# Kernel optimization log

Measured on AMD Instinct MI355X. Metric: run time of the kernel, lower is better.

## Reference

```python
import jax, jax.numpy as jnp
import numpy as np

N = 20000   # genes
E = 200000  # global edges
P = 300     # pathways
EP = 2000   # edges per pathway (global node indices)
D = 3       # in_dim == number of omics (forced by nn.Linear(3,1))


def setup_inputs():
    key = jax.random.key(0)
    ks = jax.random.split(key, 20)
    f = lambda i, shape: jax.random.normal(ks[i], shape, dtype=jnp.float32) * 0.1
    return {
        "x": f(0, (N, D)),
        "edge_index": jax.random.randint(ks[1], (2, E), 0, N),
        "path_edges": jax.random.randint(ks[2], (P, 2, EP), 0, N),
        "W_pool": f(3, (D, D)), "b_pool": f(4, (D,)),
        "W_self": f(5, (D, D)), "W_neigh": f(6, (D, D)), "b_conv": f(7, (D,)),
        "sub_Wl": f(8, (P, D, D)), "sub_bl": f(9, (P, D)), "sub_Wr": f(10, (P, D, D)),
        "pool_Wrel": f(11, (P, D, 1)), "pool_Wroot": f(12, (P, D, 1)), "pool_b": f(13, (P, 1)),
        "gate_W": f(14, (P, D, 1)), "gate_b": f(15, (P, 1)),
        "lin_W": f(16, (D, 1)), "lin_b": f(17, (1,)),
        "mlp_W": f(18, (P, 1)), "mlp_b": f(19, (1,)),
    }


def reference(x, edge_index, path_edges, W_pool, b_pool, W_self, W_neigh, b_conv,
              sub_Wl, sub_bl, sub_Wr, pool_Wrel, pool_Wroot, pool_b,
              gate_W, gate_b, lin_W, lin_b, mlp_W, mlp_b):
    n = x.shape[0]
    # add_self_loops on the global edge_index
    loops = jnp.arange(n)
    src = jnp.concatenate([edge_index[0], loops])
    dst = jnp.concatenate([edge_index[1], loops])

    # global SAGEConv with 'pool' aggregator: max_j relu(W_pool h_j), then self + neigh
    hp = jax.nn.relu(x @ W_pool + b_pool)                       # [N,D]
    agg = jax.ops.segment_max(hp[src], dst, num_segments=n)     # [N,D] (self-loops -> no empty segments)
    h = jnp.tanh(x @ W_self + agg @ W_neigh + b_conv)           # [N,D]

    k = int(np.ceil(0.8 * n))  # SAGPooling ratio=0.8 over all N nodes (full x is passed per pathway)

    def per_path(pe, Wl, bl, Wr, Wrel, Wroot, pb, gW, gb):
        s, d = pe[0], pe[1]
        # SAGEConv (mean aggr) on pathway subgraph edges over full node set
        msum = jax.ops.segment_sum(h[s], d, num_segments=n)
        cnt = jax.ops.segment_sum(jnp.ones(s.shape, h.dtype), d, num_segments=n)
        mean = msum / jnp.maximum(cnt, 1.0)[:, None]
        xc = jax.nn.relu(mean @ Wl + bl + h @ Wr)               # [N,D]
        # SAGPooling score via GraphConv (add aggr): W_rel * sum_j x_j + W_root * x + b
        asum = jax.ops.segment_sum(xc[s], d, num_segments=n)
        score = (asum @ Wrel + xc @ Wroot + pb)[:, 0]           # [N]
        topv, perm = jax.lax.top_k(score, k)
        xk = xc[perm] * jnp.tanh(topv)[:, None]                 # [k,D]
        # GlobalAttention readout: softmax gate over kept nodes
        gate = jax.nn.softmax((xk @ gW + gb)[:, 0])             # [k]
        return jax.nn.relu(gate @ xk)                            # [D]

    readout = jax.vmap(per_path)(path_edges, sub_Wl, sub_bl, sub_Wr,
                                 pool_Wrel, pool_Wroot, pool_b, gate_W, gate_b)  # [P,D]
    r = jax.nn.relu(readout @ lin_W + lin_b).T                  # [1,P]
    # mlp: Dropout (identity in eval) -> ReLU -> Linear(P,1) -> Sigmoid
    return jax.nn.sigmoid(jax.nn.relu(r) @ mlp_W + mlp_b)       # [1,1]
```

## Files before the change

### kernel.cpp

```cpp
#include <hip/hip_runtime.h>
#include <math.h>

#define MAXM 2048
#define BMW  640
#define BS   1024
#define NB   2048

__device__ __forceinline__ unsigned fkey(float f){
  unsigned u = __float_as_uint(f);
  return (u & 0x80000000u) ? ~u : (u | 0x80000000u);
}
__device__ __forceinline__ int lbin(float sc, float lo, float scl){
  int b = (int)((sc - lo) * scl);
  return b < 0 ? 0 : (b > NB-1 ? NB-1 : b);
}
__device__ __forceinline__ float fast_tanh(float x){
  float e = __expf(2.f*x);
  return 1.f - 2.f*__builtin_amdgcn_rcpf(e + 1.f);
}
__device__ __forceinline__ void hp_eval(const float* __restrict__ x, int i,
                                        const float* __restrict__ Wp,
                                        const float* __restrict__ bp, float* o){
  float x0 = x[i*3+0], x1 = x[i*3+1], x2 = x[i*3+2];
  #pragma unroll
  for (int j = 0; j < 3; ++j)
    o[j] = fmaxf(x0*Wp[0*3+j] + x1*Wp[1*3+j] + x2*Wp[2*3+j] + bp[j], 0.f);
}

__global__ void k_edge(const float* __restrict__ x, const int* __restrict__ ei,
                       const float* __restrict__ Wp, const float* __restrict__ bp,
                       float* __restrict__ agg, float* __restrict__ acc,
                       unsigned* __restrict__ counter, int E){
  if (blockIdx.x == 0 && threadIdx.x == 0){ acc[0] = 0.f; counter[0] = 0u; }
  int e = blockIdx.x*blockDim.x + threadIdx.x;
  if (e >= E) return;
  int s = ei[e], d = ei[E+e];
  float o[3]; hp_eval(x, s, Wp, bp, o);
  #pragma unroll
  for (int j = 0; j < 3; ++j)
    if (o[j] > 0.f && o[j] > agg[d*3+j])
      atomicMax((int*)&agg[d*3+j], __float_as_int(o[j]));
}

__global__ void k_h2(const float* __restrict__ x, float* __restrict__ hb,
                     const float* __restrict__ Wp, const float* __restrict__ bp,
                     const float* __restrict__ Ws, const float* __restrict__ Wn,
                     const float* __restrict__ bc, int N){
  int i = blockIdx.x*blockDim.x + threadIdx.x;
  if (i >= N) return;
  float hp[3]; hp_eval(x, i, Wp, bp, hp);
  float x0 = x[i*3+0], x1 = x[i*3+1], x2 = x[i*3+2];
  float a0 = fmaxf(hb[i*3+0], hp[0]);
  float a1 = fmaxf(hb[i*3+1], hp[1]);
  float a2 = fmaxf(hb[i*3+2], hp[2]);
  float o[3];
  #pragma unroll
  for (int j = 0; j < 3; ++j){
    float v = x0*Ws[0*3+j] + x1*Ws[1*3+j] + x2*Ws[2*3+j]
            + a0*Wn[0*3+j] + a1*Wn[1*3+j] + a2*Wn[2*3+j] + bc[j];
    o[j] = tanhf(v);
  }
  hb[i*3+0] = o[0]; hb[i*3+1] = o[1]; hb[i*3+2] = o[2];
}

__global__ void __launch_bounds__(BS)
k_mega(const float* __restrict__ h, const int* __restrict__ pe,
       const float* __restrict__ sWl, const float* __restrict__ sbl, const float* __restrict__ sWr,
       const float* __restrict__ pWrel, const float* __restrict__ pWroot, const float* __restrict__ pB,
       const float* __restrict__ gW, const float* __restrict__ gB,
       const float* __restrict__ linW, const float* __restrict__ linb,
       const float* __restrict__ mlpW, const float* __restrict__ mlpb,
       float* __restrict__ spG, float* __restrict__ acc, unsigned* __restrict__ counter,
       unsigned* __restrict__ out, int N, int EP, int K, int P){
  __shared__ unsigned bm[BMW];
  __shared__ int      wpfx[BMW];
  __shared__ float    msum[MAXM*3];
  __shared__ unsigned scrA[NB];
  __shared__ unsigned scrB[NB];
  __shared__ unsigned candIdx[NB];
  __shared__ float    wredf[(BS/64)*2];
  __shared__ float    wredA[(BS/64)*4];
  __shared__ float    wredB[(BS/64)*4];
  __shared__ float    s_mn, s_mx;
  __shared__ float    rlo[3], rsc[3];
  __shared__ int      rb[3];
  __shared__ int      s_r, s_C, s_cc, s_done, s_fused;
  __shared__ unsigned s_uT;

  const int p = blockIdx.x;
  const int tid = threadIdx.x;

  float Wl[9], Wr[9], bl[3], wrel[3], wroot[3], gw[3];
  #pragma unroll
  for (int j = 0; j < 9; ++j){ Wl[j] = sWl[p*9+j]; Wr[j] = sWr[p*9+j]; }
  #pragma unroll
  for (int j = 0; j < 3; ++j){
    bl[j] = sbl[p*3+j]; wrel[j] = pWrel[p*3+j];
    wroot[j] = pWroot[p*3+j]; gw[j] = gW[p*3+j];
  }
  float pbv = pB[p], gbv = gB[p];
  float* sp = spG + (size_t)p*N;

  int*   cnt  = (int*)scrA;
  float* adot = (float*)scrB;

  for (int s = tid; s < MAXM; s += BS){
    cnt[s] = 0; adot[s] = 0.f;
    msum[s*3+0]=0.f; msum[s*3+1]=0.f; msum[s*3+2]=0.f;
  }
  for (int s = tid; s < BMW; s += BS) bm[s] = 0u;
  if (tid == 0){ s_done = 0; s_fused = 0; s_uT = 0u; }
  __syncthreads();

  const int* ps = pe + (size_t)p*2*EP;
  const int* pd = ps + EP;

  for (int e = tid; e < EP; e += BS) atomicOr(&bm[pd[e]>>5], 1u << (pd[e]&31));
  __syncthreads();
  if (tid < 64){
    int l = tid, base = l*10;
    int c[10], s = 0;
    #pragma unroll
    for (int q = 0; q < 10; ++q){ c[q] = __popc(bm[base+q]); s += c[q]; }
    int pre = s;
    #pragma unroll
    for (int off = 1; off < 64; off <<= 1){
      int t = __shfl_up(pre, off);
      if (l >= off) pre += t;
    }
    pre -= s;
    #pragma unroll
    for (int q = 0; q < 10; ++q){ wpfx[base+q] = pre; pre += c[q]; }
  }
  __syncthreads();
  for (int e = tid; e < EP; e += BS){
    int s = ps[e], d = pd[e];
    int r = wpfx[d>>5] + __popc(bm[d>>5] & ((1u << (d&31)) - 1u));
    atomicAdd(&cnt[r], 1);
    atomicAdd(&msum[r*3+0], h[s*3+0]);
    atomicAdd(&msum[r*3+1], h[s*3+1]);
    atomicAdd(&msum[r*3+2], h[s*3+2]);
  }
  __syncthreads();
  for (int r = tid; r < MAXM; r += BS){
    int c = cnt[r];
    if (c > 0){
      float inv = 1.f / (float)c;
      msum[r*3+0] *= inv; msum[r*3+1] *= inv; msum[r*3+2] *= inv;
    }
  }
  __syncthreads();
  for (int e = tid; e < EP; e += BS){
    int s = ps[e], d = pd[e];
    float m0=0.f,m1=0.f,m2=0.f;
    unsigned w = bm[s>>5];
    if ((w >> (s&31)) & 1u){
      int rs = wpfx[s>>5] + __popc(w & ((1u << (s&31)) - 1u));
      m0 = msum[rs*3+0]; m1 = msum[rs*3+1]; m2 = msum[rs*3+2];
    }
    float h0 = h[s*3+0], h1 = h[s*3+1], h2 = h[s*3+2];
    float x0 = fmaxf(m0*Wl[0]+m1*Wl[3]+m2*Wl[6] + bl[0] + h0*Wr[0]+h1*Wr[3]+h2*Wr[6], 0.f);
    float x1 = fmaxf(m0*Wl[1]+m1*Wl[4]+m2*Wl[7] + bl[1] + h0*Wr[1]+h1*Wr[4]+h2*Wr[7], 0.f);
    float x2 = fmaxf(m0*Wl[2]+m1*Wl[5]+m2*Wl[8] + bl[2] + h0*Wr[2]+h1*Wr[5]+h2*Wr[8], 0.f);
    int rd = wpfx[d>>5] + __popc(bm[d>>5] & ((1u << (d&31)) - 1u));
    atomicAdd(&adot[rd], x0*wrel[0] + x1*wrel[1] + x2*wrel[2]);
  }
  __syncthreads();

  float mn = 3.0e38f, mx = -3.0e38f;
  float tl = 0.f, ta0 = 0.f, ta1 = 0.f, ta2 = 0.f;
  for (int i = tid; i < N; i += BS){
    float m0=0.f,m1=0.f,m2=0.f,ad=0.f;
    unsigned w = bm[i>>5];
    if ((w >> (i&31)) & 1u){
      int r = wpfx[i>>5] + __popc(w & ((1u << (i&31)) - 1u));
      m0 = msum[r*3+0]; m1 = msum[r*3+1]; m2 = msum[r*3+2];
      ad = adot[r];
    }
    float h0 = h[i*3+0], h1 = h[i*3+1], h2 = h[i*3+2];
    float x0 = fmaxf(m0*Wl[0]+m1*Wl[3]+m2*Wl[6] + bl[0] + h0*Wr[0]+h1*Wr[3]+h2*Wr[6], 0.f);
    float x1 = fmaxf(m0*Wl[1]+m1*Wl[4]+m2*Wl[7] + bl[1] + h0*Wr[1]+h1*Wr[4]+h2*Wr[7], 0.f);
    float x2 = fmaxf(m0*Wl[2]+m1*Wl[5]+m2*Wl[8] + bl[2] + h0*Wr[2]+h1*Wr[5]+h2*Wr[8], 0.f);
    float sc = ad + x0*wroot[0]+x1*wroot[1]+x2*wroot[2] + pbv;
    sp[i] = sc;
    mn = fminf(mn, sc); mx = fmaxf(mx, sc);
    float tt = fast_tanh(sc);
    float g = fminf(fmaxf(tt*(x0*gw[0]+x1*gw[1]+x2*gw[2]) + gbv, -60.f), 60.f);
    float e = __expf(g);
    float et = e * tt;
    tl += e; ta0 += et*x0; ta1 += et*x1; ta2 += et*x2;
  }
  #pragma unroll
  for (int off = 32; off > 0; off >>= 1){
    mn  = fminf(mn, __shfl_down(mn, off));
    mx  = fmaxf(mx, __shfl_down(mx, off));
    tl  += __shfl_down(tl,  off); ta0 += __shfl_down(ta0, off);
    ta1 += __shfl_down(ta1, off); ta2 += __shfl_down(ta2, off);
  }
  if ((tid & 63) == 0){
    int w = tid >> 6;
    wredf[w*2+0] = mn; wredf[w*2+1] = mx;
    wredA[w*4+0]=tl; wredA[w*4+1]=ta0; wredA[w*4+2]=ta1; wredA[w*4+3]=ta2;
  }
  __syncthreads();
  if (tid == 0){
    float a = 3.0e38f, b = -3.0e38f;
    for (int w = 0; w < BS/64; ++w){ a = fminf(a, wredf[w*2+0]); b = fmaxf(b, wredf[w*2+1]); }
    s_mn = a; s_mx = b; s_r = K;
    if (!(b > a)){ s_uT = fkey(a); s_done = 1; s_fused = 1; }
  }
  __syncthreads();

  unsigned* hist = scrA;
  unsigned* cand = scrB;

  float dl = 0.f, d0 = 0.f, d1 = 0.f, d2 = 0.f;

  for (int t = 0; t < 3; ++t){
    __syncthreads();
    if (s_done) break;
    float lo, hi;
    if (t == 0){ lo = s_mn; hi = s_mx; }
    else { lo = rlo[t-1] + rb[t-1]/rsc[t-1]; hi = rlo[t-1] + (rb[t-1]+1)/rsc[t-1]; }
    float scl = 2047.0f / (hi - lo);
    if (!(hi > lo) || !(scl < 1e37f)){
      if (tid == 0){ s_uT = fkey(lo); s_done = 1; }
      __syncthreads();
      continue;
    }
    for (int b = tid; b < NB; b += BS) hist[b] = 0u;
    __syncthreads();
    if (t == 0){
      if ((N & 3) == 0){
        int G = N >> 2;
        for (int g = tid; g < G; g += BS){
          float4 v = ((const float4*)sp)[g];
          atomicAdd(&hist[lbin(v.x, lo, scl)], 1u);
          atomicAdd(&hist[lbin(v.y, lo, scl)], 1u);
          atomicAdd(&hist[lbin(v.z, lo, scl)], 1u);
          atomicAdd(&hist[lbin(v.w, lo, scl)], 1u);
        }
      } else {
        for (int i = tid; i < N; i += BS) atomicAdd(&hist[lbin(sp[i], lo, scl)], 1u);
      }
    } else {
      for (int i = tid; i < N; i += BS){
        float sc = sp[i];
        bool act = true;
        for (int q = 0; q < t; ++q) act = act && (lbin(sc, rlo[q], rsc[q]) == rb[q]);
        if (act) atomicAdd(&hist[lbin(sc, lo, scl)], 1u);
      }
    }
    __syncthreads();
    if (tid < 64){
      int l = tid;
      unsigned s = 0;
      for (int q = 0; q < 32; ++q) s += hist[l*32+q];
      unsigned S = s;
      #pragma unroll
      for (int off = 1; off < 64; off <<= 1){
        unsigned u2 = __shfl_down(S, off);
        if (l + off < 64) S += u2;
      }
      unsigned suf = S - s;
      unsigned r = (unsigned)s_r;
      int b = -1; unsigned sufnext = 0, cb = 0;
      for (int q = 31; q >= 0; --q){
        unsigned c = hist[l*32+q];
        unsigned nsuf = suf + c;
        if (nsuf >= r && suf < r){ b = l*32+q; sufnext = suf; cb = c; }
        suf = nsuf;
      }
      if (b >= 0){
        rb[t] = b; rlo[t] = lo; rsc[t] = scl;
        s_r = (int)(r - sufnext);
        s_C = (int)cb;
      }
    }
    __syncthreads();
    int C = s_C;
    if (C <= NB){
      if (tid == 0) s_cc = 0;
      __syncthreads();
      for (int i = tid; i < N; i += BS){
        float sc = sp[i];
        bool iscand = true, isdrop = false;
        for (int q = 0; q <= t; ++q){
          int b = lbin(sc, rlo[q], rsc[q]);
          if (b != rb[q]){ iscand = false; isdrop = (b < rb[q]); break; }
        }
        if (iscand){
          int ix = atomicAdd(&s_cc, 1);
          if (ix < NB){ cand[ix] = fkey(sc); candIdx[ix] = (unsigned)i; }
        } else if (isdrop){
          float m0=0.f,m1=0.f,m2=0.f;
          unsigned w = bm[i>>5];
          if ((w >> (i&31)) & 1u){
            int r = wpfx[i>>5] + __popc(w & ((1u << (i&31)) - 1u));
            m0 = msum[r*3+0]; m1 = msum[r*3+1]; m2 = msum[r*3+2];
          }
          float h0 = h[i*3+0], h1 = h[i*3+1], h2 = h[i*3+2];
          float x0 = fmaxf(m0*Wl[0]+m1*Wl[3]+m2*Wl[6] + bl[0] + h0*Wr[0]+h1*Wr[3]+h2*Wr[6], 0.f);
          float x1 = fmaxf(m0*Wl[1]+m1*Wl[4]+m2*Wl[7] + bl[1] + h0*Wr[1]+h1*Wr[4]+h2*Wr[7], 0.f);
          float x2 = fmaxf(m0*Wl[2]+m1*Wl[5]+m2*Wl[8] + bl[2] + h0*Wr[2]+h1*Wr[5]+h2*Wr[8], 0.f);
          float tt = fast_tanh(sc);
          float g = fminf(fmaxf(tt*(x0*gw[0]+x1*gw[1]+x2*gw[2]) + gbv, -60.f), 60.f);
          float e = __expf(g);
          float et = e * tt;
          dl += e; d0 += et*x0; d1 += et*x1; d2 += et*x2;
        }
      }
      __syncthreads();
      if (tid < 64){
        int l = tid;
        unsigned pref = 0u, mask = 0u;
        int r = s_r;
        #pragma unroll
        for (int pass = 0; pass < 4; ++pass){
          int shift = 24 - 8*pass;
          hist[4*l+0]=0u; hist[4*l+1]=0u; hist[4*l+2]=0u; hist[4*l+3]=0u;
          asm volatile("s_waitcnt lgkmcnt(0)" ::: "memory");
          for (int j = l; j < C; j += 64){
            unsigned u = cand[j];
            if ((u & mask) == pref) atomicAdd(&hist[(u>>shift)&255u], 1u);
          }
          asm volatile("s_waitcnt lgkmcnt(0)" ::: "memory");
          unsigned h0 = hist[4*l+0], h1 = hist[4*l+1], h2 = hist[4*l+2], h3 = hist[4*l+3];
          unsigned ssum = h0+h1+h2+h3;
          unsigned S = ssum;
          #pragma unroll
          for (int off = 1; off < 64; off <<= 1){
            unsigned u2 = __shfl_down(S, off);
            if (l + off < 64) S += u2;
          }
          unsigned Snext = S - ssum;
          unsigned rr = (unsigned)r;
          unsigned suf3 = h3 + Snext;
          unsigned suf2 = h2 + suf3;
          unsigned suf1 = h1 + suf2;
          unsigned suf0 = h0 + suf1;
          int b = -1; unsigned sufn = 0;
          if      (suf3 >= rr && Snext < rr){ b = 4*l+3; sufn = Snext; }
          else if (suf2 >= rr && suf3  < rr){ b = 4*l+2; sufn = suf3; }
          else if (suf1 >= rr && suf2  < rr){ b = 4*l+1; sufn = suf2; }
          else if (suf0 >= rr && suf1  < rr){ b = 4*l+0; sufn = suf1; }
          unsigned long long ball = __ballot(b >= 0);
          int src = __ffsll(ball) - 1;
          b    = __shfl(b, src);
          sufn = (unsigned)__shfl((int)sufn, src);
          pref |= (unsigned)b << shift;
          mask |= 255u << shift;
          r = (int)(rr - sufn);
        }
        if (l == 0) s_uT = pref;
      }
      if (tid == 0){ s_done = 1; s_fused = 1; }
      __syncthreads();
      {
        const unsigned uTl = s_uT;
        for (int j = tid; j < C; j += BS){
          if (cand[j] < uTl){
            int i = (int)candIdx[j];
            float sc = sp[i];
            float m0=0.f,m1=0.f,m2=0.f;
            unsigned w = bm[i>>5];
            if ((w >> (i&31)) & 1u){
              int r = wpfx[i>>5] + __popc(w & ((1u << (i&31)) - 1u));
              m0 = msum[r*3+0]; m1 = msum[r*3+1]; m2 = msum[r*3+2];
            }
            float h0 = h[i*3+0], h1 = h[i*3+1], h2 = h[i*3+2];
            float x0 = fmaxf(m0*Wl[0]+m1*Wl[3]+m2*Wl[6] + bl[0] + h0*Wr[0]+h1*Wr[3]+h2*Wr[6], 0.f);
            float x1 = fmaxf(m0*Wl[1]+m1*Wl[4]+m2*Wl[7] + bl[1] + h0*Wr[1]+h1*Wr[4]+h2*Wr[7], 0.f);
            float x2 = fmaxf(m0*Wl[2]+m1*Wl[5]+m2*Wl[8] + bl[2] + h0*Wr[2]+h1*Wr[5]+h2*Wr[8], 0.f);
            float tt = fast_tanh(sc);
            float g = fminf(fmaxf(tt*(x0*gw[0]+x1*gw[1]+x2*gw[2]) + gbv, -60.f), 60.f);
            float e = __expf(g);
            float et = e * tt;
            dl += e; d0 += et*x0; d1 += et*x1; d2 += et*x2;
          }
        }
      }
    } else if (t == 2){
      if (tid == 0){ s_uT = fkey(lo + rb[t]/scl); s_done = 1; }
      __syncthreads();
    }
  }
  __syncthreads();
  const unsigned uT = s_uT;

  if (!s_fused){
    for (int i = tid; i < N; i += BS){
      float sc = sp[i];
      if (fkey(sc) < uT){
        float m0=0.f,m1=0.f,m2=0.f;
        unsigned w = bm[i>>5];
        if ((w >> (i&31)) & 1u){
          int r = wpfx[i>>5] + __popc(w & ((1u << (i&31)) - 1u));
          m0 = msum[r*3+0]; m1 = msum[r*3+1]; m2 = msum[r*3+2];
        }
        float h0 = h[i*3+0], h1 = h[i*3+1], h2 = h[i*3+2];
        float x0 = fmaxf(m0*Wl[0]+m1*Wl[3]+m2*Wl[6] + bl[0] + h0*Wr[0]+h1*Wr[3]+h2*Wr[6], 0.f);
        float x1 = fmaxf(m0*Wl[1]+m1*Wl[4]+m2*Wl[7] + bl[1] + h0*Wr[1]+h1*Wr[4]+h2*Wr[7], 0.f);
        float x2 = fmaxf(m0*Wl[2]+m1*Wl[5]+m2*Wl[8] + bl[2] + h0*Wr[2]+h1*Wr[5]+h2*Wr[8], 0.f);
        float tt = fast_tanh(sc);
        float g = fminf(fmaxf(tt*(x0*gw[0]+x1*gw[1]+x2*gw[2]) + gbv, -60.f), 60.f);
        float e = __expf(g);
        float et = e * tt;
        dl += e; d0 += et*x0; d1 += et*x1; d2 += et*x2;
      }
    }
  }
  #pragma unroll
  for (int off = 32; off > 0; off >>= 1){
    dl += __shfl_down(dl, off); d0 += __shfl_down(d0, off);
    d1 += __shfl_down(d1, off); d2 += __shfl_down(d2, off);
  }
  if ((tid & 63) == 0){
    int w = tid >> 6;
    wredB[w*4+0]=dl; wredB[w*4+1]=d0; wredB[w*4+2]=d1; wredB[w*4+3]=d2;
  }
  __syncthreads();
  if (tid == 0){
    float L=0.f, A0=0.f, A1=0.f, A2=0.f;
    for (int w = 0; w < BS/64; ++w){
      L  += wredA[w*4+0] - wredB[w*4+0];
      A0 += wredA[w*4+1] - wredB[w*4+1];
      A1 += wredA[w*4+2] - wredB[w*4+2];
      A2 += wredA[w*4+3] - wredB[w*4+3];
    }
    float inv = 1.f / L;
    float r0 = fmaxf(A0*inv, 0.f);
    float r1 = fmaxf(A1*inv, 0.f);
    float r2 = fmaxf(A2*inv, 0.f);
    float rr = fmaxf(r0*linW[0] + r1*linW[1] + r2*linW[2] + linb[0], 0.f);
    atomicAdd(acc, rr * mlpW[p]);
    __threadfence();
    unsigned old = atomicAdd(counter, 1u);
    if (old == (unsigned)(P-1)){
      __threadfence();
      float z = atomicAdd(acc, 0.f) + mlpb[0];
      float a = 1.f / (1.f + expf(-z));
      unsigned A = __float_as_uint(a);
      unsigned B = (A + 0x7FFFu + ((A >> 16) & 1u)) >> 16;
      out[0] = (A & 0xFFFF0000u) | (B & 0xFFFFu);
    }
  }
}

extern "C" void kernel_launch(void* const* d_in, const int* in_sizes, int n_in,
                              void* d_out, int out_size, void* d_ws, size_t ws_size,
                              hipStream_t stream){
  const float* x      = (const float*)d_in[0];
  const int*   ei     = (const int*)  d_in[1];
  const int*   pe     = (const int*)  d_in[2];
  const float* W_pool = (const float*)d_in[3];
  const float* b_pool = (const float*)d_in[4];
  const float* W_self = (const float*)d_in[5];
  const float* W_neigh= (const float*)d_in[6];
  const float* b_conv = (const float*)d_in[7];
  const float* sWl    = (const float*)d_in[8];
  const float* sbl    = (const float*)d_in[9];
  const float* sWr    = (const float*)d_in[10];
  const float* pWrel  = (const float*)d_in[11];
  const float* pWroot = (const float*)d_in[12];
  const float* pB     = (const float*)d_in[13];
  const float* gW     = (const float*)d_in[14];
  const float* gB     = (const float*)d_in[15];
  const float* linW   = (const float*)d_in[16];
  const float* linb   = (const float*)d_in[17];
  const float* mlpW   = (const float*)d_in[18];
  const float* mlpb   = (const float*)d_in[19];

  const int N  = in_sizes[0] / 3;
  const int E  = in_sizes[1] / 2;
  const int P  = in_sizes[13];
  const int EP = in_sizes[2] / (2 * P);
  const int K  = (4*N + 4) / 5;

  float*    ws      = (float*)d_ws;
  float*    acc     = ws;
  unsigned* counter = (unsigned*)(ws + 1);
  float*    agg     = ws + 16;
  float*    h       = agg;
  float*    spG     = ws + 16 + (size_t)3*N;

  k_edge<<<(E+255)/256, 256, 0, stream>>>(x, ei, W_pool, b_pool, agg, acc, counter, E);
  k_h2  <<<(N+255)/256, 256, 0, stream>>>(x, agg, W_pool, b_pool,
                                          W_self, W_neigh, b_conv, N);
  k_mega<<<P, BS, 0, stream>>>(h, pe, sWl, sbl, sWr, pWrel, pWroot, pB, gW, gB,
                               linW, linb, mlpW, mlpb,
                               spG, acc, counter, (unsigned*)d_out, N, EP, K, P);
}
```

Measured before the change: 236.2 us.

## Fuse all stages into one cooperative kernel with grid sync and dynamic pathway tickets

Merges the edge max-aggregation, the h computation and the per-pathway mega kernel into a single cooperative launch of 256 persistent blocks. Grid-wide syncs separate the global stages, and pathways are then handed out through an atomic ticket counter. The aim is to remove two kernel launches and the inter-kernel gaps, and to balance 300 pathways over resident blocks. The costs are grid.sync overhead, only 256 blocks doing the edge phase, and a persistent loop that runs some blocks through two pathways serially.

```diff
diff --git a/kernel.cpp b/kernel.cpp
--- a/kernel.cpp
+++ b/kernel.cpp
@@ -1,9 +1,13 @@
 #include <hip/hip_runtime.h>
+#include <hip/hip_cooperative_groups.h>
 #include <math.h>
+
+namespace cg = cooperative_groups;
 
 #define MAXM 2048
 #define BMW  640
 #define BS   1024
+#define GRID 256
 #define NB   2048
 
 __device__ __forceinline__ unsigned fkey(float f){
@@ -27,51 +31,21 @@
     o[j] = fmaxf(x0*Wp[0*3+j] + x1*Wp[1*3+j] + x2*Wp[2*3+j] + bp[j], 0.f);
 }
 
-__global__ void k_edge(const float* __restrict__ x, const int* __restrict__ ei,
-                       const float* __restrict__ Wp, const float* __restrict__ bp,
-                       float* __restrict__ agg, float* __restrict__ acc,
-                       unsigned* __restrict__ counter, int E){
-  if (blockIdx.x == 0 && threadIdx.x == 0){ acc[0] = 0.f; counter[0] = 0u; }
-  int e = blockIdx.x*blockDim.x + threadIdx.x;
-  if (e >= E) return;
-  int s = ei[e], d = ei[E+e];
-  float o[3]; hp_eval(x, s, Wp, bp, o);
-  #pragma unroll
-  for (int j = 0; j < 3; ++j)
-    if (o[j] > 0.f && o[j] > agg[d*3+j])
-      atomicMax((int*)&agg[d*3+j], __float_as_int(o[j]));
-}
-
-__global__ void k_h2(const float* __restrict__ x, float* __restrict__ hb,
-                     const float* __restrict__ Wp, const float* __restrict__ bp,
-                     const float* __restrict__ Ws, const float* __restrict__ Wn,
-                     const float* __restrict__ bc, int N){
-  int i = blockIdx.x*blockDim.x + threadIdx.x;
-  if (i >= N) return;
-  float hp[3]; hp_eval(x, i, Wp, bp, hp);
-  float x0 = x[i*3+0], x1 = x[i*3+1], x2 = x[i*3+2];
-  float a0 = fmaxf(hb[i*3+0], hp[0]);
-  float a1 = fmaxf(hb[i*3+1], hp[1]);
-  float a2 = fmaxf(hb[i*3+2], hp[2]);
-  float o[3];
-  #pragma unroll
-  for (int j = 0; j < 3; ++j){
-    float v = x0*Ws[0*3+j] + x1*Ws[1*3+j] + x2*Ws[2*3+j]
-            + a0*Wn[0*3+j] + a1*Wn[1*3+j] + a2*Wn[2*3+j] + bc[j];
-    o[j] = tanhf(v);
-  }
-  hb[i*3+0] = o[0]; hb[i*3+1] = o[1]; hb[i*3+2] = o[2];
-}
-
 __global__ void __launch_bounds__(BS)
-k_mega(const float* __restrict__ h, const int* __restrict__ pe,
-       const float* __restrict__ sWl, const float* __restrict__ sbl, const float* __restrict__ sWr,
-       const float* __restrict__ pWrel, const float* __restrict__ pWroot, const float* __restrict__ pB,
-       const float* __restrict__ gW, const float* __restrict__ gB,
-       const float* __restrict__ linW, const float* __restrict__ linb,
-       const float* __restrict__ mlpW, const float* __restrict__ mlpb,
-       float* __restrict__ spG, float* __restrict__ acc, unsigned* __restrict__ counter,
-       unsigned* __restrict__ out, int N, int EP, int K, int P){
+k_fused(const float* __restrict__ x, const int* __restrict__ ei,
+        const int* __restrict__ pe,
+        const float* __restrict__ Wp, const float* __restrict__ bp,
+        const float* __restrict__ Ws, const float* __restrict__ Wn,
+        const float* __restrict__ bc,
+        const float* __restrict__ sWl, const float* __restrict__ sbl, const float* __restrict__ sWr,
+        const float* __restrict__ pWrel, const float* __restrict__ pWroot, const float* __restrict__ pB,
+        const float* __restrict__ gW, const float* __restrict__ gB,
+        const float* __restrict__ linW, const float* __restrict__ linb,
+        const float* __restrict__ mlpW, const float* __restrict__ mlpb,
+        float* __restrict__ hbuf, float* __restrict__ spG,
+        float* __restrict__ acc, unsigned* __restrict__ counter,
+        unsigned* __restrict__ ticket, unsigned* __restrict__ out,
+        int N, int E, int EP, int K, int P){
   __shared__ unsigned bm[BMW];
   __shared__ int      wpfx[BMW];
   __shared__ float    msum[MAXM*3];
@@ -86,282 +60,254 @@
   __shared__ int      rb[3];
   __shared__ int      s_r, s_C, s_cc, s_done, s_fused;
   __shared__ unsigned s_uT;
-
-  const int p = blockIdx.x;
+  __shared__ int      s_p;
+
   const int tid = threadIdx.x;
-
-  float Wl[9], Wr[9], bl[3], wrel[3], wroot[3], gw[3];
-  #pragma unroll
-  for (int j = 0; j < 9; ++j){ Wl[j] = sWl[p*9+j]; Wr[j] = sWr[p*9+j]; }
-  #pragma unroll
-  for (int j = 0; j < 3; ++j){
-    bl[j] = sbl[p*3+j]; wrel[j] = pWrel[p*3+j];
-    wroot[j] = pWroot[p*3+j]; gw[j] = gW[p*3+j];
+  const int gtid = blockIdx.x*BS + tid;
+  const int gsz  = gridDim.x*BS;
+  cg::grid_group grid = cg::this_grid();
+
+  if (gtid == 0){ acc[0] = 0.f; counter[0] = 0u; ticket[0] = 0u; }
+  float* agg = hbuf;
+  for (int e = gtid; e < E; e += gsz){
+    int s = ei[e], d = ei[E+e];
+    float o[3]; hp_eval(x, s, Wp, bp, o);
+    #pragma unroll
+    for (int j = 0; j < 3; ++j)
+      if (o[j] > 0.f && o[j] > agg[d*3+j])
+        atomicMax((int*)&agg[d*3+j], __float_as_int(o[j]));
   }
-  float pbv = pB[p], gbv = gB[p];
-  float* sp = spG + (size_t)p*N;
-
-  int*   cnt  = (int*)scrA;
-  float* adot = (float*)scrB;
-
-  for (int s = tid; s < MAXM; s += BS){
-    cnt[s] = 0; adot[s] = 0.f;
-    msum[s*3+0]=0.f; msum[s*3+1]=0.f; msum[s*3+2]=0.f;
+  grid.sync();
+
+  for (int i = gtid; i < N; i += gsz){
+    float hp[3]; hp_eval(x, i, Wp, bp, hp);
+    float x0 = x[i*3+0], x1 = x[i*3+1], x2 = x[i*3+2];
+    float a0 = fmaxf(agg[i*3+0], hp[0]);
+    float a1 = fmaxf(agg[i*3+1], hp[1]);
+    float a2 = fmaxf(agg[i*3+2], hp[2]);
+    float o[3];
+    #pragma unroll
+    for (int j = 0; j < 3; ++j){
+      float v = x0*Ws[0*3+j] + x1*Ws[1*3+j] + x2*Ws[2*3+j]
+              + a0*Wn[0*3+j] + a1*Wn[1*3+j] + a2*Wn[2*3+j] + bc[j];
+      o[j] = tanhf(v);
+    }
+    agg[i*3+0] = o[0]; agg[i*3+1] = o[1]; agg[i*3+2] = o[2];
   }
-  for (int s = tid; s < BMW; s += BS) bm[s] = 0u;
-  if (tid == 0){ s_done = 0; s_fused = 0; s_uT = 0u; }
-  __syncthreads();
-
-  const int* ps = pe + (size_t)p*2*EP;
-  const int* pd = ps + EP;
-
-  for (int e = tid; e < EP; e += BS) atomicOr(&bm[pd[e]>>5], 1u << (pd[e]&31));
-  __syncthreads();
-  if (tid < 64){
-    int l = tid, base = l*10;
-    int c[10], s = 0;
+  grid.sync();
+
+  const float* h = hbuf;
+
+  while (true){
+    __syncthreads();
+    if (tid == 0) s_p = (int)atomicAdd(ticket, 1u);
+    __syncthreads();
+    const int p = s_p;
+    if (p >= P) break;
+
+    float Wl[9], Wr[9], bl[3], wrel[3], wroot[3], gw[3];
     #pragma unroll
-    for (int q = 0; q < 10; ++q){ c[q] = __popc(bm[base+q]); s += c[q]; }
-    int pre = s;
+    for (int j = 0; j < 9; ++j){ Wl[j] = sWl[p*9+j]; Wr[j] = sWr[p*9+j]; }
     #pragma unroll
-    for (int off = 1; off < 64; off <<= 1){
-      int t = __shfl_up(pre, off);
-      if (l >= off) pre += t;
-    }
-    pre -= s;
-    #pragma unroll
-    for (int q = 0; q < 10; ++q){ wpfx[base+q] = pre; pre += c[q]; }
-  }
-  __syncthreads();
-  for (int e = tid; e < EP; e += BS){
-    int s = ps[e], d = pd[e];
-    int r = wpfx[d>>5] + __popc(bm[d>>5] & ((1u << (d&31)) - 1u));
-    atomicAdd(&cnt[r], 1);
-    atomicAdd(&msum[r*3+0], h[s*3+0]);
-    atomicAdd(&msum[r*3+1], h[s*3+1]);
-    atomicAdd(&msum[r*3+2], h[s*3+2]);
-  }
-  __syncthreads();
-  for (int r = tid; r < MAXM; r += BS){
-    int c = cnt[r];
-    if (c > 0){
-      float inv = 1.f / (float)c;
-      msum[r*3+0] *= inv; msum[r*3+1] *= inv; msum[r*3+2] *= inv;
-    }
-  }
-  __syncthreads();
-  for (int e = tid; e < EP; e += BS){
-    int s = ps[e], d = pd[e];
-    float m0=0.f,m1=0.f,m2=0.f;
-    unsigned w = bm[s>>5];
-    if ((w >> (s&31)) & 1u){
-      int rs = wpfx[s>>5] + __popc(w & ((1u << (s&31)) - 1u));
-      m0 = msum[rs*3+0]; m1 = msum[rs*3+1]; m2 = msum[rs*3+2];
-    }
-    float h0 = h[s*3+0], h1 = h[s*3+1], h2 = h[s*3+2];
-    float x0 = fmaxf(m0*Wl[0]+m1*Wl[3]+m2*Wl[6] + bl[0] + h0*Wr[0]+h1*Wr[3]+h2*Wr[6], 0.f);
-    float x1 = fmaxf(m0*Wl[1]+m1*Wl[4]+m2*Wl[7] + bl[1] + h0*Wr[1]+h1*Wr[4]+h2*Wr[7], 0.f);
-    float x2 = fmaxf(m0*Wl[2]+m1*Wl[5]+m2*Wl[8] + bl[2] + h0*Wr[2]+h1*Wr[5]+h2*Wr[8], 0.f);
-    int rd = wpfx[d>>5] + __popc(bm[d>>5] & ((1u << (d&31)) - 1u));
-    atomicAdd(&adot[rd], x0*wrel[0] + x1*wrel[1] + x2*wrel[2]);
-  }
-  __syncthreads();
-
-  float mn = 3.0e38f, mx = -3.0e38f;
-  float tl = 0.f, ta0 = 0.f, ta1 = 0.f, ta2 = 0.f;
-  for (int i = tid; i < N; i += BS){
-    float m0=0.f,m1=0.f,m2=0.f,ad=0.f;
-    unsigned w = bm[i>>5];
-    if ((w >> (i&31)) & 1u){
-      int r = wpfx[i>>5] + __popc(w & ((1u << (i&31)) - 1u));
-      m0 = msum[r*3+0]; m1 = msum[r*3+1]; m2 = msum[r*3+2];
-      ad = adot[r];
-    }
-    float h0 = h[i*3+0], h1 = h[i*3+1], h2 = h[i*3+2];
-    float x0 = fmaxf(m0*Wl[0]+m1*Wl[3]+m2*Wl[6] + bl[0] + h0*Wr[0]+h1*Wr[3]+h2*Wr[6], 0.f);
-    float x1 = fmaxf(m0*Wl[1]+m1*Wl[4]+m2*Wl[7] + bl[1] + h0*Wr[1]+h1*Wr[4]+h2*Wr[7], 0.f);
-    float x2 = fmaxf(m0*Wl[2]+m1*Wl[5]+m2*Wl[8] + bl[2] + h0*Wr[2]+h1*Wr[5]+h2*Wr[8], 0.f);
-    float sc = ad + x0*wroot[0]+x1*wroot[1]+x2*wroot[2] + pbv;
-    sp[i] = sc;
-    mn = fminf(mn, sc); mx = fmaxf(mx, sc);
-    float tt = fast_tanh(sc);
-    float g = fminf(fmaxf(tt*(x0*gw[0]+x1*gw[1]+x2*gw[2]) + gbv, -60.f), 60.f);
-    float e = __expf(g);
-    float et = e * tt;
-    tl += e; ta0 += et*x0; ta1 += et*x1; ta2 += et*x2;
-  }
-  #pragma unroll
-  for (int off = 32; off > 0; off >>= 1){
-    mn  = fminf(mn, __shfl_down(mn, off));
-    mx  = fmaxf(mx, __shfl_down(mx, off));
-    tl  += __shfl_down(tl,  off); ta0 += __shfl_down(ta0, off);
-    ta1 += __shfl_down(ta1, off); ta2 += __shfl_down(ta2, off);
-  }
-  if ((tid & 63) == 0){
-    int w = tid >> 6;
-    wredf[w*2+0] = mn; wredf[w*2+1] = mx;
-    wredA[w*4+0]=tl; wredA[w*4+1]=ta0; wredA[w*4+2]=ta1; wredA[w*4+3]=ta2;
-  }
-  __syncthreads();
-  if (tid == 0){
-    float a = 3.0e38f, b = -3.0e38f;
-    for (int w = 0; w < BS/64; ++w){ a = fminf(a, wredf[w*2+0]); b = fmaxf(b, wredf[w*2+1]); }
-    s_mn = a; s_mx = b; s_r = K;
-    if (!(b > a)){ s_uT = fkey(a); s_done = 1; s_fused = 1; }
-  }
-  __syncthreads();
-
-  unsigned* hist = scrA;
-  unsigned* cand = scrB;
-
-  float dl = 0.f, d0 = 0.f, d1 = 0.f, d2 = 0.f;
-
-  for (int t = 0; t < 3; ++t){
-    __syncthreads();
-    if (s_done) break;
-    float lo, hi;
-    if (t == 0){ lo = s_mn; hi = s_mx; }
-    else { lo = rlo[t-1] + rb[t-1]/rsc[t-1]; hi = rlo[t-1] + (rb[t-1]+1)/rsc[t-1]; }
-    float scl = 2047.0f / (hi - lo);
-    if (!(hi > lo) || !(scl < 1e37f)){
-      if (tid == 0){ s_uT = fkey(lo); s_done = 1; }
-      __syncthreads();
-      continue;
-    }
-    for (int b = tid; b < NB; b += BS) hist[b] = 0u;
-    __syncthreads();
-    if (t == 0){
-      if ((N & 3) == 0){
-        int G = N >> 2;
-        for (int g = tid; g < G; g += BS){
-          float4 v = ((const float4*)sp)[g];
-          atomicAdd(&hist[lbin(v.x, lo, scl)], 1u);
-          atomicAdd(&hist[lbin(v.y, lo, scl)], 1u);
-          atomicAdd(&hist[lbin(v.z, lo, scl)], 1u);
-          atomicAdd(&hist[lbin(v.w, lo, scl)], 1u);
-        }
-      } else {
-        for (int i = tid; i < N; i += BS) atomicAdd(&hist[lbin(sp[i], lo, scl)], 1u);
-      }
-    } else {
-      for (int i = tid; i < N; i += BS){
-        float sc = sp[i];
-        bool act = true;
-        for (int q = 0; q < t; ++q) act = act && (lbin(sc, rlo[q], rsc[q]) == rb[q]);
-        if (act) atomicAdd(&hist[lbin(sc, lo, scl)], 1u);
-      }
-    }
+    for (int j = 0; j < 3; ++j){
+      bl[j] = sbl[p*3+j]; wrel[j] = pWrel[p*3+j];
+      wroot[j] = pWroot[p*3+j]; gw[j] = gW[p*3+j];
+    }
+    float pbv = pB[p], gbv = gB[p];
+    float* sp = spG + (size_t)p*N;
+
+    int*   cnt  = (int*)scrA;
+    float* adot = (float*)scrB;
+
+    for (int s = tid; s < MAXM; s += BS){
+      cnt[s] = 0; adot[s] = 0.f;
+      msum[s*3+0]=0.f; msum[s*3+1]=0.f; msum[s*3+2]=0.f;
+    }
+    for (int s = tid; s < BMW; s += BS) bm[s] = 0u;
+    if (tid == 0){ s_done = 0; s_fused = 0; s_uT = 0u; }
+    __syncthreads();
+
+    const int* ps = pe + (size_t)p*2*EP;
+    const int* pd = ps + EP;
+
+    for (int e = tid; e < EP; e += BS) atomicOr(&bm[pd[e]>>5], 1u << (pd[e]&31));
     __syncthreads();
     if (tid < 64){
-      int l = tid;
-      unsigned s = 0;
-      for (int q = 0; q < 32; ++q) s += hist[l*32+q];
-      unsigned S = s;
+      int l = tid, base = l*10;
+      int c[10], s = 0;
+      #pragma unroll
+      for (int q = 0; q < 10; ++q){ c[q] = __popc(bm[base+q]); s += c[q]; }
+      int pre = s;
       #pragma unroll
       for (int off = 1; off < 64; off <<= 1){
-        unsigned u2 = __shfl_down(S, off);
-        if (l + off < 64) S += u2;
-      }
-      unsigned suf = S - s;
-      unsigned r = (unsigned)s_r;
-      int b = -1; unsigned sufnext = 0, cb = 0;
-      for (int q = 31; q >= 0; --q){
-        unsigned c = hist[l*32+q];
-        unsigned nsuf = suf + c;
-        if (nsuf >= r && suf < r){ b = l*32+q; sufnext = suf; cb = c; }
-        suf = nsuf;
-      }
-      if (b >= 0){
-        rb[t] = b; rlo[t] = lo; rsc[t] = scl;
-        s_r = (int)(r - sufnext);
-        s_C = (int)cb;
-      }
-    }
-    __syncthreads();
-    int C = s_C;
-    if (C <= NB){
-      if (tid == 0) s_cc = 0;
+        int t = __shfl_up(pre, off);
+        if (l >= off) pre += t;
+      }
+      pre -= s;
+      #pragma unroll
+      for (int q = 0; q < 10; ++q){ wpfx[base+q] = pre; pre += c[q]; }
+    }
+    __syncthreads();
+    for (int e = tid; e < EP; e += BS){
+      int s = ps[e], d = pd[e];
+      int r = wpfx[d>>5] + __popc(bm[d>>5] & ((1u << (d&31)) - 1u));
+      atomicAdd(&cnt[r], 1);
+      atomicAdd(&msum[r*3+0], h[s*3+0]);
+      atomicAdd(&msum[r*3+1], h[s*3+1]);
+      atomicAdd(&msum[r*3+2], h[s*3+2]);
+    }
+    __syncthreads();
+    for (int r = tid; r < MAXM; r += BS){
+      int c = cnt[r];
+      if (c > 0){
+        float inv = 1.f / (float)c;
+        msum[r*3+0] *= inv; msum[r*3+1] *= inv; msum[r*3+2] *= inv;
+      }
+    }
+    __syncthreads();
+    for (int e = tid; e < EP; e += BS){
+      int s = ps[e], d = pd[e];
+      float m0=0.f,m1=0.f,m2=0.f;
+      unsigned w = bm[s>>5];
+      if ((w >> (s&31)) & 1u){
+        int rs = wpfx[s>>5] + __popc(w & ((1u << (s&31)) - 1u));
+        m0 = msum[rs*3+0]; m1 = msum[rs*3+1]; m2 = msum[rs*3+2];
+      }
+      float h0 = h[s*3+0], h1 = h[s*3+1], h2 = h[s*3+2];
+      float x0 = fmaxf(m0*Wl[0]+m1*Wl[3]+m2*Wl[6] + bl[0] + h0*Wr[0]+h1*Wr[3]+h2*Wr[6], 0.f);
+      float x1 = fmaxf(m0*Wl[1]+m1*Wl[4]+m2*Wl[7] + bl[1] + h0*Wr[1]+h1*Wr[4]+h2*Wr[7], 0.f);
+      float x2 = fmaxf(m0*Wl[2]+m1*Wl[5]+m2*Wl[8] + bl[2] + h0*Wr[2]+h1*Wr[5]+h2*Wr[8], 0.f);
+      int rd = wpfx[d>>5] + __popc(bm[d>>5] & ((1u << (d&31)) - 1u));
+      atomicAdd(&adot[rd], x0*wrel[0] + x1*wrel[1] + x2*wrel[2]);
+    }
+    __syncthreads();
+
+    float mn = 3.0e38f, mx = -3.0e38f;
+    float tl = 0.f, ta0 = 0.f, ta1 = 0.f, ta2 = 0.f;
+    for (int i = tid; i < N; i += BS){
+      float m0=0.f,m1=0.f,m2=0.f,ad=0.f;
+      unsigned w = bm[i>>5];
+      if ((w >> (i&31)) & 1u){
+        int r = wpfx[i>>5] + __popc(w & ((1u << (i&31)) - 1u));
+        m0 = msum[r*3+0]; m1 = msum[r*3+1]; m2 = msum[r*3+2];
+        ad = adot[r];
+      }
+      float h0 = h[i*3+0], h1 = h[i*3+1], h2 = h[i*3+2];
+      float x0 = fmaxf(m0*Wl[0]+m1*Wl[3]+m2*Wl[6] + bl[0] + h0*Wr[0]+h1*Wr[3]+h2*Wr[6], 0.f);
+      float x1 = fmaxf(m0*Wl[1]+m1*Wl[4]+m2*Wl[7] + bl[1] + h0*Wr[1]+h1*Wr[4]+h2*Wr[7], 0.f);
+      float x2 = fmaxf(m0*Wl[2]+m1*Wl[5]+m2*Wl[8] + bl[2] + h0*Wr[2]+h1*Wr[5]+h2*Wr[8], 0.f);
+      float sc = ad + x0*wroot[0]+x1*wroot[1]+x2*wroot[2] + pbv;
+      sp[i] = sc;
+      mn = fminf(mn, sc); mx = fmaxf(mx, sc);
+      float tt = fast_tanh(sc);
+      float g = fminf(fmaxf(tt*(x0*gw[0]+x1*gw[1]+x2*gw[2]) + gbv, -60.f), 60.f);
+      float e = __expf(g);
+      float et = e * tt;
+      tl += e; ta0 += et*x0; ta1 += et*x1; ta2 += et*x2;
+    }
+    #pragma unroll
+    for (int off = 32; off > 0; off >>= 1){
+      mn  = fminf(mn, __shfl_down(mn, off));
+      mx  = fmaxf(mx, __shfl_down(mx, off));
+      tl  += __shfl_down(tl,  off); ta0 += __shfl_down(ta0, off);
+      ta1 += __shfl_down(ta1, off); ta2 += __shfl_down(ta2, off);
+    }
+    if ((tid & 63) == 0){
+      int w = tid >> 6;
+      wredf[w*2+0] = mn; wredf[w*2+1] = mx;
+      wredA[w*4+0]=tl; wredA[w*4+1]=ta0; wredA[w*4+2]=ta1; wredA[w*4+3]=ta2;
+    }
+    __syncthreads();
+    if (tid == 0){
+      float a = 3.0e38f, b = -3.0e38f;
+      for (int w = 0; w < BS/64; ++w){ a = fminf(a, wredf[w*2+0]); b = fmaxf(b, wredf[w*2+1]); }
+      s_mn = a; s_mx = b; s_r = K;
+      if (!(b > a)){ s_uT = fkey(a); s_done = 1; s_fused = 1; }
+    }
+    __syncthreads();
+
+    unsigned* hist = scrA;
+    unsigned* cand = scrB;
+
+    float dl = 0.f, d0 = 0.f, d1 = 0.f, d2 = 0.f;
+
+    for (int t = 0; t < 3; ++t){
       __syncthreads();
-      for (int i = tid; i < N; i += BS){
-        float sc = sp[i];
-        bool iscand = true, isdrop = false;
-        for (int q = 0; q <= t; ++q){
-          int b = lbin(sc, rlo[q], rsc[q]);
-          if (b != rb[q]){ iscand = false; isdrop = (b < rb[q]); break; }
-        }
-        if (iscand){
-          int ix = atomicAdd(&s_cc, 1);
-          if (ix < NB){ cand[ix] = fkey(sc); candIdx[ix] = (unsigned)i; }
-        } else if (isdrop){
-          float m0=0.f,m1=0.f,m2=0.f;
-          unsigned w = bm[i>>5];
-          if ((w >> (i&31)) & 1u){
-            int r = wpfx[i>>5] + __popc(w & ((1u << (i&31)) - 1u));
-            m0 = msum[r*3+0]; m1 = msum[r*3+1]; m2 = msum[r*3+2];
+      if (s_done) break;
+      float lo, hi;
+      if (t == 0){ lo = s_mn; hi = s_mx; }
+      else { lo = rlo[t-1] + rb[t-1]/rsc[t-1]; hi = rlo[t-1] + (rb[t-1]+1)/rsc[t-1]; }
+      float scl = 2047.0f / (hi - lo);
+      if (!(hi > lo) || !(scl < 1e37f)){
+        if (tid == 0){ s_uT = fkey(lo); s_done = 1; }
+        __syncthreads();
+        continue;
+      }
+      for (int b = tid; b < NB; b += BS) hist[b] = 0u;
+      __syncthreads();
+      if (t == 0){
+        if ((N & 3) == 0){
+          int G = N >> 2;
+          for (int g = tid; g < G; g += BS){
+            float4 v = ((const float4*)sp)[g];
+            atomicAdd(&hist[lbin(v.x, lo, scl)], 1u);
+            atomicAdd(&hist[lbin(v.y, lo, scl)], 1u);
+            atomicAdd(&hist[lbin(v.z, lo, scl)], 1u);
+            atomicAdd(&hist[lbin(v.w, lo, scl)], 1u);
           }
-          float h0 = h[i*3+0], h1 = h[i*3+1], h2 = h[i*3+2];
-          float x0 = fmaxf(m0*Wl[0]+m1*Wl[3]+m2*Wl[6] + bl[0] + h0*Wr[0]+h1*Wr[3]+h2*Wr[6], 0.f);
-          float x1 = fmaxf(m0*Wl[1]+m1*Wl[4]+m2*Wl[7] + bl[1] + h0*Wr[1]+h1*Wr[4]+h2*Wr[7], 0.f);
-          float x2 = fmaxf(m0*Wl[2]+m1*Wl[5]+m2*Wl[8] + bl[2] + h0*Wr[2]+h1*Wr[5]+h2*Wr[8], 0.f);
-          float tt = fast_tanh(sc);
-          float g = fminf(fmaxf(tt*(x0*gw[0]+x1*gw[1]+x2*gw[2]) + gbv, -60.f), 60.f);
-          float e = __expf(g);
-          float et = e * tt;
-          dl += e; d0 += et*x0; d1 += et*x1; d2 += et*x2;
+        } else {
+          for (int i = tid; i < N; i += BS) atomicAdd(&hist[lbin(sp[i], lo, scl)], 1u);
+        }
+      } else {
+        for (int i = tid; i < N; i += BS){
+          float sc = sp[i];
+          bool act = true;
+          for (int q = 0; q < t; ++q) act = act && (lbin(sc, rlo[q], rsc[q]) == rb[q]);
+          if (act) atomicAdd(&hist[lbin(sc, lo, scl)], 1u);
         }
       }
       __syncthreads();
       if (tid < 64){
         int l = tid;
-        unsigned pref = 0u, mask = 0u;
-        int r = s_r;
+        unsigned s = 0;
+        for (int q = 0; q < 32; ++q) s += hist[l*32+q];
+        unsigned S = s;
         #pragma unroll
-        for (int pass = 0; pass < 4; ++pass){
-          int shift = 24 - 8*pass;
-          hist[4*l+0]=0u; hist[4*l+1]=0u; hist[4*l+2]=0u; hist[4*l+3]=0u;
-          asm volatile("s_waitcnt lgkmcnt(0)" ::: "memory");
-          for (int j = l; j < C; j += 64){
-            unsigned u = cand[j];
-            if ((u & mask) == pref) atomicAdd(&hist[(u>>shift)&255u], 1u);
+        for (int off = 1; off < 64; off <<= 1){
+          unsigned u2 = __shfl_down(S, off);
+          if (l + off < 64) S += u2;
+        }
+        unsigned suf = S - s;
+        unsigned r = (unsigned)s_r;
+        int b = -1; unsigned sufnext = 0, cb = 0;
+        for (int q = 31; q >= 0; --q){
+          unsigned c = hist[l*32+q];
+          unsigned nsuf = suf + c;
+          if (nsuf >= r && suf < r){ b = l*32+q; sufnext = suf; cb = c; }
+          suf = nsuf;
+        }
+        if (b >= 0){
+          rb[t] = b; rlo[t] = lo; rsc[t] = scl;
+          s_r = (int)(r - sufnext);
+          s_C = (int)cb;
+        }
+      }
+      __syncthreads();
+      int C = s_C;
+      if (C <= NB){
+        if (tid == 0) s_cc = 0;
+        __syncthreads();
+        for (int i = tid; i < N; i += BS){
+          float sc = sp[i];
+          bool iscand = true, isdrop = false;
+          for (int q = 0; q <= t; ++q){
+            int b = lbin(sc, rlo[q], rsc[q]);
+            if (b != rb[q]){ iscand = false; isdrop = (b < rb[q]); break; }
           }
-          asm volatile("s_waitcnt lgkmcnt(0)" ::: "memory");
-          unsigned h0 = hist[4*l+0], h1 = hist[4*l+1], h2 = hist[4*l+2], h3 = hist[4*l+3];
-          unsigned ssum = h0+h1+h2+h3;
-          unsigned S = ssum;
-          #pragma unroll
-          for (int off = 1; off < 64; off <<= 1){
-            unsigned u2 = __shfl_down(S, off);
-            if (l + off < 64) S += u2;
-          }
-          unsigned Snext = S - ssum;
-          unsigned rr = (unsigned)r;
-          unsigned suf3 = h3 + Snext;
-          unsigned suf2 = h2 + suf3;
-          unsigned suf1 = h1 + suf2;
-          unsigned suf0 = h0 + suf1;
-          int b = -1; unsigned sufn = 0;
-          if      (suf3 >= rr && Snext < rr){ b = 4*l+3; sufn = Snext; }
-          else if (suf2 >= rr && suf3  < rr){ b = 4*l+2; sufn = suf3; }
-          else if (suf1 >= rr && suf2  < rr){ b = 4*l+1; sufn = suf2; }
-          else if (suf0 >= rr && suf1  < rr){ b = 4*l+0; sufn = suf1; }
-          unsigned long long ball = __ballot(b >= 0);
-          int src = __ffsll(ball) - 1;
-          b    = __shfl(b, src);
-          sufn = (unsigned)__shfl((int)sufn, src);
-          pref |= (unsigned)b << shift;
-          mask |= 255u << shift;
-          r = (int)(rr - sufn);
-        }
-        if (l == 0) s_uT = pref;
-      }
-      if (tid == 0){ s_done = 1; s_fused = 1; }
-      __syncthreads();
-      {
-        const unsigned uTl = s_uT;
-        for (int j = tid; j < C; j += BS){
-          if (cand[j] < uTl){
-            int i = (int)candIdx[j];
-            float sc = sp[i];
+          if (iscand){
+            int ix = atomicAdd(&s_cc, 1);
+            if (ix < NB){ cand[ix] = fkey(sc); candIdx[ix] = (unsigned)i; }
+          } else if (isdrop){
             float m0=0.f,m1=0.f,m2=0.f;
             unsigned w = bm[i>>5];
             if ((w >> (i&31)) & 1u){
@@ -379,70 +325,140 @@
             dl += e; d0 += et*x0; d1 += et*x1; d2 += et*x2;
           }
         }
-      }
-    } else if (t == 2){
-      if (tid == 0){ s_uT = fkey(lo + rb[t]/scl); s_done = 1; }
-      __syncthreads();
-    }
-  }
-  __syncthreads();
-  const unsigned uT = s_uT;
-
-  if (!s_fused){
-    for (int i = tid; i < N; i += BS){
-      float sc = sp[i];
-      if (fkey(sc) < uT){
-        float m0=0.f,m1=0.f,m2=0.f;
-        unsigned w = bm[i>>5];
-        if ((w >> (i&31)) & 1u){
-          int r = wpfx[i>>5] + __popc(w & ((1u << (i&31)) - 1u));
-          m0 = msum[r*3+0]; m1 = msum[r*3+1]; m2 = msum[r*3+2];
-        }
-        float h0 = h[i*3+0], h1 = h[i*3+1], h2 = h[i*3+2];
-        float x0 = fmaxf(m0*Wl[0]+m1*Wl[3]+m2*Wl[6] + bl[0] + h0*Wr[0]+h1*Wr[3]+h2*Wr[6], 0.f);
-        float x1 = fmaxf(m0*Wl[1]+m1*Wl[4]+m2*Wl[7] + bl[1] + h0*Wr[1]+h1*Wr[4]+h2*Wr[7], 0.f);
-        float x2 = fmaxf(m0*Wl[2]+m1*Wl[5]+m2*Wl[8] + bl[2] + h0*Wr[2]+h1*Wr[5]+h2*Wr[8], 0.f);
-        float tt = fast_tanh(sc);
-        float g = fminf(fmaxf(tt*(x0*gw[0]+x1*gw[1]+x2*gw[2]) + gbv, -60.f), 60.f);
-        float e = __expf(g);
-        float et = e * tt;
-        dl += e; d0 += et*x0; d1 += et*x1; d2 += et*x2;
-      }
-    }
-  }
-  #pragma unroll
-  for (int off = 32; off > 0; off >>= 1){
-    dl += __shfl_down(dl, off); d0 += __shfl_down(d0, off);
-    d1 += __shfl_down(d1, off); d2 += __shfl_down(d2, off);
-  }
-  if ((tid & 63) == 0){
-    int w = tid >> 6;
-    wredB[w*4+0]=dl; wredB[w*4+1]=d0; wredB[w*4+2]=d1; wredB[w*4+3]=d2;
-  }
-  __syncthreads();
-  if (tid == 0){
-    float L=0.f, A0=0.f, A1=0.f, A2=0.f;
-    for (int w = 0; w < BS/64; ++w){
-      L  += wredA[w*4+0] - wredB[w*4+0];
-      A0 += wredA[w*4+1] - wredB[w*4+1];
-      A1 += wredA[w*4+2] - wredB[w*4+2];
-      A2 += wredA[w*4+3] - wredB[w*4+3];
-    }
-    float inv = 1.f / L;
-    float r0 = fmaxf(A0*inv, 0.f);
-    float r1 = fmaxf(A1*inv, 0.f);
-    float r2 = fmaxf(A2*inv, 0.f);
-    float rr = fmaxf(r0*linW[0] + r1*linW[1] + r2*linW[2] + linb[0], 0.f);
-    atomicAdd(acc, rr * mlpW[p]);
-    __threadfence();
-    unsigned old = atomicAdd(counter, 1u);
-    if (old == (unsigned)(P-1)){
+        __syncthreads();
+        if (tid < 64){
+          int l = tid;
+          unsigned pref = 0u, mask = 0u;
+          int r = s_r;
+          #pragma unroll
+          for (int pass = 0; pass < 4; ++pass){
+            int shift = 24 - 8*pass;
+            hist[4*l+0]=0u; hist[4*l+1]=0u; hist[4*l+2]=0u; hist[4*l+3]=0u;
+            asm volatile("s_waitcnt lgkmcnt(0)" ::: "memory");
+            for (int j = l; j < C; j += 64){
+              unsigned u = cand[j];
+              if ((u & mask) == pref) atomicAdd(&hist[(u>>shift)&255u], 1u);
+            }
+            asm volatile("s_waitcnt lgkmcnt(0)" ::: "memory");
+            unsigned h0 = hist[4*l+0], h1 = hist[4*l+1], h2 = hist[4*l+2], h3 = hist[4*l+3];
+            unsigned ssum = h0+h1+h2+h3;
+            unsigned S = ssum;
+            #pragma unroll
+            for (int off = 1; off < 64; off <<= 1){
+              unsigned u2 = __shfl_down(S, off);
+              if (l + off < 64) S += u2;
+            }
+            unsigned Snext = S - ssum;
+            unsigned rr = (unsigned)r;
+            unsigned suf3 = h3 + Snext;
+            unsigned suf2 = h2 + suf3;
+            unsigned suf1 = h1 + suf2;
+            unsigned suf0 = h0 + suf1;
+            int b = -1; unsigned sufn = 0;
+            if      (suf3 >= rr && Snext < rr){ b = 4*l+3; sufn = Snext; }
+            else if (suf2 >= rr && suf3  < rr){ b = 4*l+2; sufn = suf3; }
+            else if (suf1 >= rr && suf2  < rr){ b = 4*l+1; sufn = suf2; }
+            else if (suf0 >= rr && suf1  < rr){ b = 4*l+0; sufn = suf1; }
+            unsigned long long ball = __ballot(b >= 0);
+            int src = __ffsll(ball) - 1;
+            b    = __shfl(b, src);
+            sufn = (unsigned)__shfl((int)sufn, src);
+            pref |= (unsigned)b << shift;
+            mask |= 255u << shift;
+            r = (int)(rr - sufn);
+          }
+          if (l == 0) s_uT = pref;
+        }
+        if (tid == 0){ s_done = 1; s_fused = 1; }
+        __syncthreads();
+        {
+          const unsigned uTl = s_uT;
+          for (int j = tid; j < C; j += BS){
+            if (cand[j] < uTl){
+              int i = (int)candIdx[j];
+              float sc = sp[i];
+              float m0=0.f,m1=0.f,m2=0.f;
+              unsigned w = bm[i>>5];
+              if ((w >> (i&31)) & 1u){
+                int r = wpfx[i>>5] + __popc(w & ((1u << (i&31)) - 1u));
+                m0 = msum[r*3+0]; m1 = msum[r*3+1]; m2 = msum[r*3+2];
+              }
+              float h0 = h[i*3+0], h1 = h[i*3+1], h2 = h[i*3+2];
+              float x0 = fmaxf(m0*Wl[0]+m1*Wl[3]+m2*Wl[6] + bl[0] + h0*Wr[0]+h1*Wr[3]+h2*Wr[6], 0.f);
+              float x1 = fmaxf(m0*Wl[1]+m1*Wl[4]+m2*Wl[7] + bl[1] + h0*Wr[1]+h1*Wr[4]+h2*Wr[7], 0.f);
+              float x2 = fmaxf(m0*Wl[2]+m1*Wl[5]+m2*Wl[8] + bl[2] + h0*Wr[2]+h1*Wr[5]+h2*Wr[8], 0.f);
+              float tt = fast_tanh(sc);
+              float g = fminf(fmaxf(tt*(x0*gw[0]+x1*gw[1]+x2*gw[2]) + gbv, -60.f), 60.f);
+              float e = __expf(g);
+              float et = e * tt;
+              dl += e; d0 += et*x0; d1 += et*x1; d2 += et*x2;
+            }
+          }
+        }
+      } else if (t == 2){
+        if (tid == 0){ s_uT = fkey(lo + rb[t]/scl); s_done = 1; }
+        __syncthreads();
+      }
+    }
+    __syncthreads();
+    const unsigned uT = s_uT;
+
+    if (!s_fused){
+      for (int i = tid; i < N; i += BS){
+        float sc = sp[i];
+        if (fkey(sc) < uT){
+          float m0=0.f,m1=0.f,m2=0.f;
+          unsigned w = bm[i>>5];
+          if ((w >> (i&31)) & 1u){
+            int r = wpfx[i>>5] + __popc(w & ((1u << (i&31)) - 1u));
+            m0 = msum[r*3+0]; m1 = msum[r*3+1]; m2 = msum[r*3+2];
+          }
+          float h0 = h[i*3+0], h1 = h[i*3+1], h2 = h[i*3+2];
+          float x0 = fmaxf(m0*Wl[0]+m1*Wl[3]+m2*Wl[6] + bl[0] + h0*Wr[0]+h1*Wr[3]+h2*Wr[6], 0.f);
+          float x1 = fmaxf(m0*Wl[1]+m1*Wl[4]+m2*Wl[7] + bl[1] + h0*Wr[1]+h1*Wr[4]+h2*Wr[7], 0.f);
+          float x2 = fmaxf(m0*Wl[2]+m1*Wl[5]+m2*Wl[8] + bl[2] + h0*Wr[2]+h1*Wr[5]+h2*Wr[8], 0.f);
+          float tt = fast_tanh(sc);
+          float g = fminf(fmaxf(tt*(x0*gw[0]+x1*gw[1]+x2*gw[2]) + gbv, -60.f), 60.f);
+          float e = __expf(g);
+          float et = e * tt;
+          dl += e; d0 += et*x0; d1 += et*x1; d2 += et*x2;
+        }
+      }
+    }
+    #pragma unroll
+    for (int off = 32; off > 0; off >>= 1){
+      dl += __shfl_down(dl, off); d0 += __shfl_down(d0, off);
+      d1 += __shfl_down(d1, off); d2 += __shfl_down(d2, off);
+    }
+    if ((tid & 63) == 0){
+      int w = tid >> 6;
+      wredB[w*4+0]=dl; wredB[w*4+1]=d0; wredB[w*4+2]=d1; wredB[w*4+3]=d2;
+    }
+    __syncthreads();
+    if (tid == 0){
+      float L=0.f, A0=0.f, A1=0.f, A2=0.f;
+      for (int w = 0; w < BS/64; ++w){
+        L  += wredA[w*4+0] - wredB[w*4+0];
+        A0 += wredA[w*4+1] - wredB[w*4+1];
+        A1 += wredA[w*4+2] - wredB[w*4+2];
+        A2 += wredA[w*4+3] - wredB[w*4+3];
+      }
+      float inv = 1.f / L;
+      float r0 = fmaxf(A0*inv, 0.f);
+      float r1 = fmaxf(A1*inv, 0.f);
+      float r2 = fmaxf(A2*inv, 0.f);
+      float rr = fmaxf(r0*linW[0] + r1*linW[1] + r2*linW[2] + linb[0], 0.f);
+      atomicAdd(acc, rr * mlpW[p]);
       __threadfence();
-      float z = atomicAdd(acc, 0.f) + mlpb[0];
-      float a = 1.f / (1.f + expf(-z));
-      unsigned A = __float_as_uint(a);
-      unsigned B = (A + 0x7FFFu + ((A >> 16) & 1u)) >> 16;
-      out[0] = (A & 0xFFFF0000u) | (B & 0xFFFFu);
+      unsigned old = atomicAdd(counter, 1u);
+      if (old == (unsigned)(P-1)){
+        __threadfence();
+        float z = atomicAdd(acc, 0.f) + mlpb[0];
+        float a = 1.f / (1.f + expf(-z));
+        unsigned A = __float_as_uint(a);
+        unsigned B = (A + 0x7FFFu + ((A >> 16) & 1u)) >> 16;
+        out[0] = (A & 0xFFFF0000u) | (B & 0xFFFFu);
+      }
     }
   }
 }
@@ -471,23 +487,30 @@
   const float* mlpW   = (const float*)d_in[18];
   const float* mlpb   = (const float*)d_in[19];
 
-  const int N  = in_sizes[0] / 3;
-  const int E  = in_sizes[1] / 2;
-  const int P  = in_sizes[13];
-  const int EP = in_sizes[2] / (2 * P);
-  const int K  = (4*N + 4) / 5;
+  int N  = in_sizes[0] / 3;
+  int E  = in_sizes[1] / 2;
+  int P  = in_sizes[13];
+  int EP = in_sizes[2] / (2 * P);
+  int K  = (4*N + 4) / 5;
 
   float*    ws      = (float*)d_ws;
   float*    acc     = ws;
   unsigned* counter = (unsigned*)(ws + 1);
-  float*    agg     = ws + 16;
-  float*    h       = agg;
+  unsigned* ticket  = (unsigned*)(ws + 2);
+  float*    hbuf    = ws + 16;
   float*    spG     = ws + 16 + (size_t)3*N;
-
-  k_edge<<<(E+255)/256, 256, 0, stream>>>(x, ei, W_pool, b_pool, agg, acc, counter, E);
-  k_h2  <<<(N+255)/256, 256, 0, stream>>>(x, agg, W_pool, b_pool,
-                                          W_self, W_neigh, b_conv, N);
-  k_mega<<<P, BS, 0, stream>>>(h, pe, sWl, sbl, sWr, pWrel, pWroot, pB, gW, gB,
-                               linW, linb, mlpW, mlpb,
-                               spG, acc, counter, (unsigned*)d_out, N, EP, K, P);
+  unsigned* outp    = (unsigned*)d_out;
+
+  void* args[] = {
+    (void*)&x, (void*)&ei, (void*)&pe,
+    (void*)&W_pool, (void*)&b_pool, (void*)&W_self, (void*)&W_neigh, (void*)&b_conv,
+    (void*)&sWl, (void*)&sbl, (void*)&sWr,
+    (void*)&pWrel, (void*)&pWroot, (void*)&pB,
+    (void*)&gW, (void*)&gB, (void*)&linW, (void*)&linb,
+    (void*)&mlpW, (void*)&mlpb,
+    (void*)&hbuf, (void*)&spG, (void*)&acc, (void*)&counter, (void*)&ticket,
+    (void*)&outp, (void*)&N, (void*)&E, (void*)&EP, (void*)&K, (void*)&P
+  };
+  hipLaunchCooperativeKernel((const void*)k_fused, dim3(GRID), dim3(BS),
+                             args, 0, stream);
 }
```

Measured after the change: 327.1 us. 1.38x slower.
